# Kernel optimization log

Hardware: AMD Instinct MI355X
Metric: run time of the kernel (lower is better)

## Reference

```python
import jax, jax.numpy as jnp
import numpy as np
import math

D, H, S, B, E, FF = 768, 12, 1024, 2, 32768, 4 * 768
HD = D // H


def layer_norm(x, g, b, eps=1e-5):
    m = jnp.mean(x, axis=-1, keepdims=True)
    v = jnp.mean((x - m) ** 2, axis=-1, keepdims=True)
    return (x - m) / jnp.sqrt(v + eps) * g + b


def setup_inputs() -> dict:
    key = jax.random.key(0)
    ks = jax.random.split(key, 24)
    w = lambda k, shape: jax.random.normal(k, shape, dtype=jnp.float32) * 0.02
    inp = {
        "x": jax.random.normal(ks[0], (B, S, D), dtype=jnp.float32),
        "adj_mask": jax.random.randint(ks[1], (B, S, S), 0, 2).astype(bool),
        "edge_attr": jax.random.normal(ks[2], (E,), dtype=jnp.float32),
        "edge_index": jax.random.randint(ks[3], (2, E), 0, S),
        "norm1_g": jnp.ones((D,), jnp.float32),
        "norm1_b": jnp.zeros((D,), jnp.float32),
        "Wq": w(ks[4], (D, D)), "bq": jnp.zeros((D,), jnp.float32),
        "Wk": w(ks[5], (D, D)), "bk": jnp.zeros((D,), jnp.float32),
        "Wv": w(ks[6], (D, D)), "bv": jnp.zeros((D,), jnp.float32),
        "Wo": w(ks[7], (D, D)), "bo": jnp.zeros((D,), jnp.float32),
        "norm2_g": jnp.ones((D,), jnp.float32),
        "norm2_b": jnp.zeros((D,), jnp.float32),
        "mlp_W1": w(ks[8], (D, FF)), "mlp_b1": jnp.zeros((FF,), jnp.float32),
        "mlp_W2": w(ks[9], (FF, D)), "mlp_b2": jnp.zeros((D,), jnp.float32),
        # per-head edge-attr MLP: Linear(1,16) -> GELU -> Linear(16,1), stacked over H heads
        "ep_W1": w(ks[10], (H, 16)), "ep_b1": jnp.zeros((H, 16), jnp.float32),
        "ep_W2": w(ks[11], (H, 16)), "ep_b2": jnp.zeros((H,), jnp.float32),
    }
    return inp


def reference(x, adj_mask, edge_attr, edge_index,
              norm1_g, norm1_b, Wq, bq, Wk, bk, Wv, bv, Wo, bo,
              norm2_g, norm2_b, mlp_W1, mlp_b1, mlp_W2, mlp_b2,
              ep_W1, ep_b1, ep_W2, ep_b2):
    Bb, Ss, Dd = x.shape
    Hh = ep_W1.shape[0]
    hd = Dd // Hh
    residual = x
    nx = layer_norm(x, norm1_g, norm1_b)
    q = (nx @ Wq + bq).reshape(Bb, Ss, Hh, hd).transpose(0, 2, 1, 3)  # [B,H,S,hd]
    k = (nx @ Wk + bk).reshape(Bb, Ss, Hh, hd).transpose(0, 2, 1, 3)
    v = (nx @ Wv + bv).reshape(Bb, Ss, Hh, hd).transpose(0, 2, 1, 3)
    scores = jnp.einsum('bhqd,bhkd->bhqk', q, k) / math.sqrt(hd)
    mask = adj_mask.astype(bool)[:, None]  # [B,1,S,S]
    scores = jnp.where(mask, scores, jnp.float32(-1e9))
    # per-edge per-head bias (computed under no_grad in the original -> stop_gradient)
    h1 = jax.nn.gelu(edge_attr[:, None, None] * ep_W1[None] + ep_b1[None], approximate=False)  # [E,H,16]
    proj = jnp.einsum('ehk,hk->eh', h1, ep_W2) + ep_b2  # [E,H]
    proj = jax.lax.stop_gradient(proj)
    src, dst = edge_index[0], edge_index[1]
    bias = jnp.zeros((Hh, Ss, Ss), x.dtype).at[:, src, dst].set(proj.T)  # [H,S,S]
    scores = scores + jnp.where(mask, bias[None], jnp.float32(0.0))
    attn = jax.nn.softmax(scores, axis=-1)
    out = jnp.einsum('bhqk,bhkd->bhqd', attn, v)
    out = out.transpose(0, 2, 1, 3).reshape(Bb, Ss, Dd)
    x = residual + (out @ Wo + bo)
    y = layer_norm(x, norm2_g, norm2_b)
    y = jax.nn.gelu(y @ mlp_W1 + mlp_b1, approximate=False) @ mlp_W2 + mlp_b2
    return x + y
```

## Files before the change

### kernel.cpp

```cpp
#include <hip/hip_runtime.h>
#include <hip/hip_bf16.h>

#define B_ 2
#define S_ 1024
#define D_ 768
#define H_ 12
#define HD_ 64
#define FF_ 3072
#define E_ 32768
#define QS_ 2304
#define NSPLIT 4
#define BHS (B_ * H_ * S_)

typedef short bf16x8 __attribute__((ext_vector_type(8)));
typedef float f32x4 __attribute__((ext_vector_type(4)));

#define SW(row, seg) ((((seg) ^ ((row) & 7)) * 8))

__device__ __forceinline__ unsigned short f2bf(float f) {
    __hip_bfloat16 h = __float2bfloat16(f);
    return __builtin_bit_cast(unsigned short, h);
}
__device__ __forceinline__ float bf2f(unsigned short u) {
    unsigned int v = ((unsigned int)u) << 16;
    return __builtin_bit_cast(float, v);
}
__device__ __forceinline__ float gelu_exact(float x) {
    return 0.5f * x * (1.0f + erff(x * 0.70710678118654752f));
}

__global__ __launch_bounds__(256) void fill_winner_kernel(int* __restrict__ winner)
{
    const int idx = (blockIdx.x * 256 + threadIdx.x) * 4;
    int4 v; v.x = -1; v.y = -1; v.z = -1; v.w = -1;
    *reinterpret_cast<int4*>(&winner[idx]) = v;
}

__global__ __launch_bounds__(256) void ln_kernel(
    const float* __restrict__ x, const float* __restrict__ g,
    const float* __restrict__ b, unsigned short* __restrict__ out)
{
    const int row = blockIdx.x;
    const int t = threadIdx.x;
    const float* xr = x + (size_t)row * D_;
    float v0 = xr[t], v1 = xr[t + 256], v2 = xr[t + 512];
    float s = v0 + v1 + v2, s2 = v0 * v0 + v1 * v1 + v2 * v2;
    for (int m = 32; m; m >>= 1) { s += __shfl_xor(s, m); s2 += __shfl_xor(s2, m); }
    __shared__ float red[8];
    const int w = t >> 6;
    if ((t & 63) == 0) { red[w] = s; red[4 + w] = s2; }
    __syncthreads();
    s = red[0] + red[1] + red[2] + red[3];
    s2 = red[4] + red[5] + red[6] + red[7];
    const float mean = s * (1.f / D_);
    const float var = s2 * (1.f / D_) - mean * mean;
    const float rstd = rsqrtf(var + 1e-5f);
    unsigned short* orow = out + (size_t)row * D_;
    orow[t]       = f2bf((v0 - mean) * rstd * g[t]       + b[t]);
    orow[t + 256] = f2bf((v1 - mean) * rstd * g[t + 256] + b[t + 256]);
    orow[t + 512] = f2bf((v2 - mean) * rstd * g[t + 512] + b[t + 512]);
}

__global__ __launch_bounds__(256) void wtrans_all_kernel(
    const float* __restrict__ Wq, const float* __restrict__ Wk, const float* __restrict__ Wv,
    const float* __restrict__ Wo, const float* __restrict__ W1, const float* __restrict__ W2,
    unsigned short* __restrict__ wqkvt, unsigned short* __restrict__ wot,
    unsigned short* __restrict__ w1t, unsigned short* __restrict__ w2t,
    const float* __restrict__ bq, const float* __restrict__ bk, const float* __restrict__ bv,
    float* __restrict__ bqkv)
{
    const int z = blockIdx.z;
    const float* src; unsigned short* dst; int K, N, nb, kb;
    if (z < 4) {
        if (blockIdx.x >= 24 || blockIdx.y >= 24) return;
        K = 768; N = 768; nb = blockIdx.x * 32; kb = blockIdx.y * 32;
        src = (z == 0) ? Wq : (z == 1) ? Wk : (z == 2) ? Wv : Wo;
        dst = (z == 3) ? wot : wqkvt + (size_t)z * 768 * 768;
    } else if (z == 4) {
        if (blockIdx.y >= 24) return;
        K = 768; N = 3072; nb = blockIdx.x * 32; kb = blockIdx.y * 32;
        src = W1; dst = w1t;
    } else {
        if (blockIdx.y >= 24) return;
        K = 3072; N = 768; nb = blockIdx.y * 32; kb = blockIdx.x * 32;
        src = W2; dst = w2t;
    }
    __shared__ float tile[32][33];
    const int tx = threadIdx.x & 31, ty = threadIdx.x >> 5;
    for (int r = 0; r < 32; r += 8)
        tile[ty + r][tx] = src[(size_t)(kb + ty + r) * N + nb + tx];
    __syncthreads();
    for (int r = 0; r < 32; r += 8)
        dst[(size_t)(nb + ty + r) * K + kb + tx] = f2bf(tile[tx][ty + r]);
    if (z == 0 && blockIdx.x == 0 && blockIdx.y == 0) {
        for (int i = threadIdx.x; i < QS_; i += 256)
            bqkv[i] = (i < 768) ? bq[i] : (i < 1536) ? bk[i - 768] : bv[i - 1536];
    }
}

template<bool RES, bool OUTBF>
__global__ __launch_bounds__(256) void gemm_kernel(
    const unsigned short* __restrict__ A, const unsigned short* __restrict__ Bt,
    const float* __restrict__ bias, const float* __restrict__ res,
    void* __restrict__ outp, int M, int N, int K)
{
    __shared__ unsigned short As[64][40];
    __shared__ unsigned short Bs[64][40];
    const int m0 = blockIdx.y * 64, n0 = blockIdx.x * 64;
    const int t = threadIdx.x;
    const int w = t >> 6, l = t & 63;
    const int wm = w >> 1, wn = w & 1;
    const int r = l & 15, g = l >> 4;
    const int srow = t >> 2, sseg = t & 3;
    f32x4 acc[2][2] = {};
    for (int k0 = 0; k0 < K; k0 += 32) {
        __syncthreads();
        const uint4 av = *reinterpret_cast<const uint4*>(A + (size_t)(m0 + srow) * K + k0 + sseg * 8);
        *reinterpret_cast<uint4*>(&As[srow][sseg * 8]) = av;
        const uint4 bv = *reinterpret_cast<const uint4*>(Bt + (size_t)(n0 + srow) * K + k0 + sseg * 8);
        *reinterpret_cast<uint4*>(&Bs[srow][sseg * 8]) = bv;
        __syncthreads();
        bf16x8 af[2], bfr[2];
        af[0]  = *reinterpret_cast<const bf16x8*>(&As[wm * 32 + r][g * 8]);
        af[1]  = *reinterpret_cast<const bf16x8*>(&As[wm * 32 + 16 + r][g * 8]);
        bfr[0] = *reinterpret_cast<const bf16x8*>(&Bs[wn * 32 + r][g * 8]);
        bfr[1] = *reinterpret_cast<const bf16x8*>(&Bs[wn * 32 + 16 + r][g * 8]);
        for (int m = 0; m < 2; m++)
            for (int n = 0; n < 2; n++)
                acc[m][n] = __builtin_amdgcn_mfma_f32_16x16x32_bf16(af[m], bfr[n], acc[m][n], 0, 0, 0);
    }
    for (int m = 0; m < 2; m++)
        for (int n = 0; n < 2; n++) {
            const int col = n0 + wn * 32 + n * 16 + r;
            const float bvv = bias[col];
            for (int j = 0; j < 4; j++) {
                const int row = m0 + wm * 32 + m * 16 + g * 4 + j;
                float v = acc[m][n][j] + bvv;
                if (RES) v += res[(size_t)row * N + col];
                if (OUTBF) ((unsigned short*)outp)[(size_t)row * N + col] = f2bf(v);
                else       ((float*)outp)[(size_t)row * N + col] = v;
            }
        }
}

__global__ __launch_bounds__(256) void gemm_splitk_kernel(
    const unsigned short* __restrict__ A, const unsigned short* __restrict__ Bt,
    float* __restrict__ part, int M, int N, int K, int klen)
{
    __shared__ unsigned short As[64][40];
    __shared__ unsigned short Bs[64][40];
    const int m0 = blockIdx.y * 64, n0 = blockIdx.x * 64;
    const int kbeg = blockIdx.z * klen;
    const int t = threadIdx.x;
    const int w = t >> 6, l = t & 63;
    const int wm = w >> 1, wn = w & 1;
    const int r = l & 15, g = l >> 4;
    const int srow = t >> 2, sseg = t & 3;
    f32x4 acc[2][2] = {};
    for (int k0 = kbeg; k0 < kbeg + klen; k0 += 32) {
        __syncthreads();
        const uint4 av = *reinterpret_cast<const uint4*>(A + (size_t)(m0 + srow) * K + k0 + sseg * 8);
        *reinterpret_cast<uint4*>(&As[srow][sseg * 8]) = av;
        const uint4 bv = *reinterpret_cast<const uint4*>(Bt + (size_t)(n0 + srow) * K + k0 + sseg * 8);
        *reinterpret_cast<uint4*>(&Bs[srow][sseg * 8]) = bv;
        __syncthreads();
        bf16x8 af[2], bfr[2];
        af[0]  = *reinterpret_cast<const bf16x8*>(&As[wm * 32 + r][g * 8]);
        af[1]  = *reinterpret_cast<const bf16x8*>(&As[wm * 32 + 16 + r][g * 8]);
        bfr[0] = *reinterpret_cast<const bf16x8*>(&Bs[wn * 32 + r][g * 8]);
        bfr[1] = *reinterpret_cast<const bf16x8*>(&Bs[wn * 32 + 16 + r][g * 8]);
        for (int m = 0; m < 2; m++)
            for (int n = 0; n < 2; n++)
                acc[m][n] = __builtin_amdgcn_mfma_f32_16x16x32_bf16(af[m], bfr[n], acc[m][n], 0, 0, 0);
    }
    float* op = part + (size_t)blockIdx.z * M * N;
    for (int m = 0; m < 2; m++)
        for (int n = 0; n < 2; n++) {
            const int col = n0 + wn * 32 + n * 16 + r;
            for (int j = 0; j < 4; j++) {
                const int row = m0 + wm * 32 + m * 16 + g * 4 + j;
                op[(size_t)row * N + col] = acc[m][n][j];
            }
        }
}

__global__ __launch_bounds__(256) void w2_reduce_kernel(
    const float* __restrict__ part, const float* __restrict__ x2,
    const float* __restrict__ b2, float* __restrict__ out)
{
    const int idx = (blockIdx.x * 256 + threadIdx.x) * 4;
    const int col = idx % D_;
    const float4 p0 = *reinterpret_cast<const float4*>(&part[idx]);
    const float4 p1 = *reinterpret_cast<const float4*>(&part[(size_t)B_ * S_ * D_ + idx]);
    const float4 xr = *reinterpret_cast<const float4*>(&x2[idx]);
    const float4 bb = *reinterpret_cast<const float4*>(&b2[col]);
    float4 o;
    o.x = xr.x + bb.x + p0.x + p1.x;
    o.y = xr.y + bb.y + p0.y + p1.y;
    o.z = xr.z + bb.z + p0.z + p1.z;
    o.w = xr.w + bb.w + p0.w + p1.w;
    *reinterpret_cast<float4*>(&out[idx]) = o;
}

template<bool GELU, bool OUTBF>
__global__ __launch_bounds__(256) void gemm128_kernel(
    const unsigned short* __restrict__ A, const unsigned short* __restrict__ Bt,
    const float* __restrict__ bias, void* __restrict__ outp,
    int M, int N, int K, int scale_below)
{
    __shared__ unsigned short As[128][64];
    __shared__ unsigned short Bs[128][64];
    const int m0 = blockIdx.y * 128, n0 = blockIdx.x * 128;
    const int t = threadIdx.x;
    const int w = t >> 6, l = t & 63;
    const int wm = w >> 1, wn = w & 1;
    const int lr = l & 15, g = l >> 4;
    f32x4 acc[4][4] = {};
    for (int k0 = 0; k0 < K; k0 += 64) {
        __syncthreads();
        for (int i = 0; i < 4; i++) {
            const int idx = i * 256 + t;
            const int row = idx >> 3, seg = idx & 7;
            *reinterpret_cast<uint4*>(&As[row][SW(row, seg)]) =
                *reinterpret_cast<const uint4*>(A + (size_t)(m0 + row) * K + k0 + seg * 8);
            *reinterpret_cast<uint4*>(&Bs[row][SW(row, seg)]) =
                *reinterpret_cast<const uint4*>(Bt + (size_t)(n0 + row) * K + k0 + seg * 8);
        }
        __syncthreads();
        for (int kk = 0; kk < 2; kk++) {
            bf16x8 af[4], bfr[4];
            for (int m = 0; m < 4; m++) {
                const int r = wm * 64 + m * 16 + lr;
                af[m] = *reinterpret_cast<const bf16x8*>(&As[r][SW(r, kk * 4 + g)]);
            }
            for (int n = 0; n < 4; n++) {
                const int r = wn * 64 + n * 16 + lr;
                bfr[n] = *reinterpret_cast<const bf16x8*>(&Bs[r][SW(r, kk * 4 + g)]);
            }
            for (int m = 0; m < 4; m++)
                for (int n = 0; n < 4; n++)
                    acc[m][n] = __builtin_amdgcn_mfma_f32_16x16x32_bf16(af[m], bfr[n], acc[m][n], 0, 0, 0);
        }
    }
    for (int m = 0; m < 4; m++)
        for (int n = 0; n < 4; n++) {
            const int col = n0 + wn * 64 + n * 16 + lr;
            const float scl = (col < scale_below) ? 0.125f : 1.0f;
            const float bvv = bias[col];
            for (int j = 0; j < 4; j++) {
                const int row = m0 + wm * 64 + m * 16 + g * 4 + j;
                float v = (acc[m][n][j] + bvv) * scl;
                if (GELU) v = gelu_exact(v);
                if (OUTBF) ((unsigned short*)outp)[(size_t)row * N + col] = f2bf(v);
                else       ((float*)outp)[(size_t)row * N + col] = v;
            }
        }
}

__global__ __launch_bounds__(256) void vtrans_kernel(
    const unsigned short* __restrict__ qkv, unsigned short* __restrict__ vt)
{
    __shared__ unsigned short T[64][68];
    const int t = threadIdx.x;
    const int s0 = blockIdx.x * 64;
    const int h = blockIdx.y, b = blockIdx.z;
    const int r = t >> 2, seg = t & 3;
    const unsigned short* src = qkv + (size_t)(b * S_ + s0 + r) * QS_ + 1536 + h * HD_ + seg * 16;
    *reinterpret_cast<uint4*>(&T[r][seg * 16])     = *reinterpret_cast<const uint4*>(src);
    *reinterpret_cast<uint4*>(&T[r][seg * 16 + 8]) = *reinterpret_cast<const uint4*>(src + 8);
    __syncthreads();
    unsigned short tmp[16];
    for (int i = 0; i < 16; i++) tmp[i] = T[seg * 16 + i][r];
    unsigned short* dst = vt + ((size_t)(b * H_ + h) * HD_ + r) * S_ + s0 + seg * 16;
    *reinterpret_cast<uint4*>(dst)     = *reinterpret_cast<uint4*>(&tmp[0]);
    *reinterpret_cast<uint4*>(dst + 8) = *reinterpret_cast<uint4*>(&tmp[8]);
}

__global__ __launch_bounds__(256) void edge_proj_scatter_kernel(
    const float* __restrict__ ea, const float* __restrict__ W1, const float* __restrict__ b1,
    const float* __restrict__ W2, const float* __restrict__ b2,
    const int* __restrict__ ei, float* __restrict__ proj, int* __restrict__ winner)
{
    const int tid = blockIdx.x * 256 + threadIdx.x;
    const int e = tid / H_, h = tid - e * H_;
    const float a = ea[e];
    float s = 0.f;
    for (int j = 0; j < 16; j++) {
        const float tv = a * W1[h * 16 + j] + b1[h * 16 + j];
        s += gelu_exact(tv) * W2[h * 16 + j];
    }
    proj[tid] = s + b2[h];
    if (h == 0) {
        const int sn = ei[e], dn = ei[E_ + e];
        atomicMax(&winner[sn * S_ + dn], e);
    }
}

__global__ __launch_bounds__(256) void ebias_kernel(
    const int* __restrict__ winner, const float* __restrict__ proj,
    unsigned short* __restrict__ ebias)
{
    const int q = blockIdx.x;
    const int t = threadIdx.x;
    const int k4 = t * 4;
    const int4 wv = *reinterpret_cast<const int4*>(&winner[q * S_ + k4]);
    for (int h = 0; h < H_; h++) {
        unsigned int lo = 0, hi = 0;
        if (wv.x >= 0) lo |= (unsigned int)f2bf(proj[(size_t)wv.x * H_ + h]);
        if (wv.y >= 0) lo |= ((unsigned int)f2bf(proj[(size_t)wv.y * H_ + h])) << 16;
        if (wv.z >= 0) hi |= (unsigned int)f2bf(proj[(size_t)wv.z * H_ + h]);
        if (wv.w >= 0) hi |= ((unsigned int)f2bf(proj[(size_t)wv.w * H_ + h])) << 16;
        uint2 val; val.x = lo; val.y = hi;
        *reinterpret_cast<uint2*>(&ebias[((size_t)h * S_ + q) * S_ + k4]) = val;
    }
}

__global__ __launch_bounds__(256) void maskpack_kernel(
    const void* __restrict__ adj, unsigned int* __restrict__ mp)
{
    __shared__ unsigned int words[32];
    __shared__ int u8f;
    const int q = blockIdx.x, b = blockIdx.y;
    const int t = threadIdx.x;
    if (t < 32) words[t] = 0;
    if (t == 0) u8f = 0;
    __syncthreads();
    const unsigned int* row8 = (const unsigned int*)((const unsigned char*)adj + ((size_t)b * S_ + q) * S_);
    const unsigned int* row32 = (const unsigned int*)((const int*)adj + ((size_t)b * S_ + q) * S_);
    const unsigned int v = row8[t];
    if (v & 0xFF00FF00u) atomicOr(&u8f, 1);
    __syncthreads();
    if (u8f) {
        unsigned int nib = 0;
        if (v & 0x000000FFu) nib |= 1u;
        if (v & 0x0000FF00u) nib |= 2u;
        if (v & 0x00FF0000u) nib |= 4u;
        if (v & 0xFF000000u) nib |= 8u;
        if (nib) atomicOr(&words[t >> 3], nib << ((t & 7) * 4));
    } else {
        for (int i = 0; i < 4; i++) {
            const int k = i * 256 + t;
            if (row32[k]) atomicOr(&words[k >> 5], 1u << (k & 31));
        }
    }
    __syncthreads();
    if (t < 32) mp[((size_t)b * S_ + q) * 32 + t] = words[t];
}

__global__ __launch_bounds__(256) void attn_mfma_kernel(
    const unsigned short* __restrict__ qkv,
    const unsigned short* __restrict__ vt,
    const unsigned short* __restrict__ ebias,
    const unsigned int* __restrict__ mp,
    float* __restrict__ pacc,
    float2* __restrict__ pml)
{
    __shared__ unsigned short Ks[64][64];
    __shared__ unsigned short Vs[64][64];
    __shared__ unsigned short Eb[64][72];
    __shared__ unsigned int   Mw[64][2];
    __shared__ unsigned short Ps[4][16][64];
    const int t = threadIdx.x;
    const int w = t >> 6, l = t & 63;
    const int lr = l & 15, g = l >> 4;
    const int qt = blockIdx.x & 15, sp = blockIdx.x >> 4;
    const int q0 = qt * 64;
    const int h = blockIdx.y, b = blockIdx.z;
    const int bh = b * H_ + h;
    const size_t qbase = (size_t)b * S_ * QS_ + h * HD_;
    const size_t kbase = qbase + 768;
    const size_t vtbase = (size_t)bh * HD_ * S_;

    const int qrow = q0 + w * 16 + lr;
    const bf16x8 af0 = *reinterpret_cast<const bf16x8*>(qkv + qbase + (size_t)qrow * QS_ + g * 8);
    const bf16x8 af1 = *reinterpret_cast<const bf16x8*>(qkv + qbase + (size_t)qrow * QS_ + 32 + g * 8);

    float m_run[4], l_run[4];
    f32x4 acc[4] = {};
    for (int j = 0; j < 4; j++) { m_run[j] = -3.0e38f; l_run[j] = 0.f; }

    const int srow = t >> 2, sseg = t & 3;
    const int kt_beg = sp * (S_ / NSPLIT), kt_end = kt_beg + S_ / NSPLIT;
    for (int kt = kt_beg; kt < kt_end; kt += 64) {
        __syncthreads();
        {
            const unsigned short* ksrc = qkv + kbase + (size_t)(kt + srow) * QS_ + sseg * 16;
            *reinterpret_cast<uint4*>(&Ks[srow][SW(srow, sseg * 2)])     = *reinterpret_cast<const uint4*>(ksrc);
            *reinterpret_cast<uint4*>(&Ks[srow][SW(srow, sseg * 2 + 1)]) = *reinterpret_cast<const uint4*>(ksrc + 8);
            const unsigned short* vsrc = vt + vtbase + (size_t)srow * S_ + kt + sseg * 16;
            *reinterpret_cast<uint4*>(&Vs[srow][SW(srow, sseg * 2)])     = *reinterpret_cast<const uint4*>(vsrc);
            *reinterpret_cast<uint4*>(&Vs[srow][SW(srow, sseg * 2 + 1)]) = *reinterpret_cast<const uint4*>(vsrc + 8);
            const unsigned short* esrc = ebias + ((size_t)h * S_ + q0 + srow) * S_ + kt + sseg * 16;
            *reinterpret_cast<uint4*>(&Eb[srow][sseg * 16])     = *reinterpret_cast<const uint4*>(esrc);
            *reinterpret_cast<uint4*>(&Eb[srow][sseg * 16 + 8]) = *reinterpret_cast<const uint4*>(esrc + 8);
            if (t < 128) Mw[t >> 1][t & 1] = mp[((size_t)b * S_ + q0 + (t >> 1)) * 32 + (kt >> 5) + (t & 1)];
        }
        __syncthreads();
        f32x4 sc[4];
        for (int n = 0; n < 4; n++) {
            const int r = n * 16 + lr;
            const bf16x8 b0 = *reinterpret_cast<const bf16x8*>(&Ks[r][SW(r, g)]);
            const bf16x8 b1 = *reinterpret_cast<const bf16x8*>(&Ks[r][SW(r, 4 + g)]);
            f32x4 z = {};
            z = __builtin_amdgcn_mfma_f32_16x16x32_bf16(af0, b0, z, 0, 0, 0);
            z = __builtin_amdgcn_mfma_f32_16x16x32_bf16(af1, b1, z, 0, 0, 0);
            sc[n] = z;
        }
        float tmax[4] = {-3.0e38f, -3.0e38f, -3.0e38f, -3.0e38f};
        for (int n = 0; n < 4; n++) {
            for (int j = 0; j < 4; j++) {
                const int rq = w * 16 + g * 4 + j;
                const unsigned int word = Mw[rq][n >> 1];
                const bool msk = (word >> ((n & 1) * 16 + lr)) & 1;
                float sval;
                if (msk) sval = sc[n][j] + bf2f(Eb[rq][n * 16 + lr]);
                else sval = -1e9f;
                sc[n][j] = sval;
                tmax[j] = fmaxf(tmax[j], sval);
            }
        }
        float pscale[4];
        for (int j = 0; j < 4; j++) {
            float tm = tmax[j];
            tm = fmaxf(tm, __shfl_xor(tm, 1));
            tm = fmaxf(tm, __shfl_xor(tm, 2));
            tm = fmaxf(tm, __shfl_xor(tm, 4));
            tm = fmaxf(tm, __shfl_xor(tm, 8));
            const float mnew = fmaxf(m_run[j], tm);
            pscale[j] = __expf(m_run[j] - mnew);
            m_run[j] = mnew;
            l_run[j] *= pscale[j];
        }
        float psum[4] = {0.f, 0.f, 0.f, 0.f};
        for (int n = 0; n < 4; n++) {
            for (int j = 0; j < 4; j++) {
                const float p = __expf(sc[n][j] - m_run[j]);
                psum[j] += p;
                const int row = g * 4 + j;
                Ps[w][row][SW(row, n * 2 + (lr >> 3)) + (lr & 7)] = f2bf(p);
            }
        }
        for (int j = 0; j < 4; j++) {
            float s = psum[j];
            s += __shfl_xor(s, 1); s += __shfl_xor(s, 2);
            s += __shfl_xor(s, 4); s += __shfl_xor(s, 8);
            l_run[j] += s;
            for (int n2 = 0; n2 < 4; n2++) acc[n2][j] *= pscale[j];
        }
        const bf16x8 pa0 = *reinterpret_cast<const bf16x8*>(&Ps[w][lr][SW(lr, g)]);
        const bf16x8 pa1 = *reinterpret_cast<const bf16x8*>(&Ps[w][lr][SW(lr, 4 + g)]);
        for (int n2 = 0; n2 < 4; n2++) {
            const int r = n2 * 16 + lr;
            const bf16x8 vb0 = *reinterpret_cast<const bf16x8*>(&Vs[r][SW(r, g)]);
            const bf16x8 vb1 = *reinterpret_cast<const bf16x8*>(&Vs[r][SW(r, 4 + g)]);
            acc[n2] = __builtin_amdgcn_mfma_f32_16x16x32_bf16(pa0, vb0, acc[n2], 0, 0, 0);
            acc[n2] = __builtin_amdgcn_mfma_f32_16x16x32_bf16(pa1, vb1, acc[n2], 0, 0, 0);
        }
    }
    const size_t prow = (size_t)sp * BHS + (size_t)bh * S_;
    for (int j = 0; j < 4; j++) {
        const int qg = q0 + w * 16 + g * 4 + j;
        for (int n2 = 0; n2 < 4; n2++)
            pacc[(prow + qg) * 64 + n2 * 16 + lr] = acc[n2][j];
        if (lr == 0) { float2 v; v.x = m_run[j]; v.y = l_run[j]; pml[prow + qg] = v; }
    }
}

__global__ __launch_bounds__(256) void attn_combine_kernel(
    const float* __restrict__ pacc, const float2* __restrict__ pml,
    unsigned short* __restrict__ attnb)
{
    const int idx = (blockIdx.x * 256 + threadIdx.x) * 4;
    const int r = idx >> 6, d = idx & 63;
    float2 ml[NSPLIT];
    float mx = -3.0e38f;
    for (int s = 0; s < NSPLIT; s++) {
        ml[s] = pml[(size_t)s * BHS + r];
        mx = fmaxf(mx, ml[s].x);
    }
    float wgt[NSPLIT], L = 0.f;
    for (int s = 0; s < NSPLIT; s++) {
        wgt[s] = __expf(ml[s].x - mx);
        L += ml[s].y * wgt[s];
    }
    const float inv = (L > 0.f) ? 1.f / L : 0.f;
    float4 o = {0.f, 0.f, 0.f, 0.f};
    for (int s = 0; s < NSPLIT; s++) {
        const float4 a = *reinterpret_cast<const float4*>(&pacc[((size_t)s * BHS + r) * 64 + d]);
        o.x += a.x * wgt[s]; o.y += a.y * wgt[s];
        o.z += a.z * wgt[s]; o.w += a.w * wgt[s];
    }
    const int bh = r >> 10, q = r & 1023;
    const int b = bh / H_, h = bh - b * H_;
    ushort4 ov;
    ov.x = f2bf(o.x * inv); ov.y = f2bf(o.y * inv);
    ov.z = f2bf(o.z * inv); ov.w = f2bf(o.w * inv);
    *reinterpret_cast<ushort4*>(&attnb[((size_t)(b * S_ + q)) * D_ + h * HD_ + d]) = ov;
}

extern "C" void kernel_launch(void* const* d_in, const int* in_sizes, int n_in,
                              void* d_out, int out_size, void* d_ws, size_t ws_size,
                              hipStream_t stream)
{
    const float* x    = (const float*)d_in[0];
    const void*  adj  = d_in[1];
    const float* ea   = (const float*)d_in[2];
    const int*   ei   = (const int*)d_in[3];
    const float* g1   = (const float*)d_in[4];
    const float* bn1  = (const float*)d_in[5];
    const float* Wq   = (const float*)d_in[6];
    const float* bq   = (const float*)d_in[7];
    const float* Wk   = (const float*)d_in[8];
    const float* bk   = (const float*)d_in[9];
    const float* Wv   = (const float*)d_in[10];
    const float* bv   = (const float*)d_in[11];
    const float* Wo   = (const float*)d_in[12];
    const float* bo   = (const float*)d_in[13];
    const float* g2   = (const float*)d_in[14];
    const float* bn2  = (const float*)d_in[15];
    const float* W1   = (const float*)d_in[16];
    const float* mb1  = (const float*)d_in[17];
    const float* W2   = (const float*)d_in[18];
    const float* mb2  = (const float*)d_in[19];
    const float* epW1 = (const float*)d_in[20];
    const float* epb1 = (const float*)d_in[21];
    const float* epW2 = (const float*)d_in[22];
    const float* epb2 = (const float*)d_in[23];

    char* ws = (char*)d_ws;
    size_t off = 0;
    auto carve = [&](size_t bytes) -> void* {
        void* p = ws + off;
        off += (bytes + 255) & ~(size_t)255;
        return p;
    };
    unsigned short* wqkvt = (unsigned short*)carve((size_t)QS_ * D_ * 2);
    unsigned short* wot   = (unsigned short*)carve((size_t)D_ * D_ * 2);
    unsigned short* w1t   = (unsigned short*)carve((size_t)FF_ * D_ * 2);
    unsigned short* w2t   = (unsigned short*)carve((size_t)D_ * FF_ * 2);
    float*          bqkv  = (float*)carve((size_t)QS_ * 4);
    float*          proj  = (float*)carve((size_t)E_ * H_ * 4);
    int*            winner= (int*)carve((size_t)S_ * S_ * 4);
    unsigned short* ebias = (unsigned short*)carve((size_t)H_ * S_ * S_ * 2);
    unsigned int*   mpk   = (unsigned int*)carve((size_t)B_ * S_ * 32 * 4);
    unsigned short* nxb   = (unsigned short*)carve((size_t)B_ * S_ * D_ * 2);
    unsigned short* attnb = (unsigned short*)carve((size_t)B_ * S_ * D_ * 2);
    unsigned short* qkv   = (unsigned short*)carve((size_t)B_ * S_ * QS_ * 2);
    unsigned short* vtb   = (unsigned short*)carve((size_t)B_ * S_ * D_ * 2);
    float*          x2f   = (float*)carve((size_t)B_ * S_ * D_ * 4);
    float*          pacc  = (float*)carve((size_t)NSPLIT * BHS * 64 * 4);
    float2*         pml   = (float2*)carve((size_t)NSPLIT * BHS * 8);
    unsigned short* ln2b = nxb;
    unsigned short* hb   = qkv;
    float*          pw2  = (float*)ebias;

    const int M = B_ * S_;

    fill_winner_kernel<<<(S_ * S_) / 1024, 256, 0, stream>>>(winner);

    wtrans_all_kernel<<<dim3(96, 24, 6), 256, 0, stream>>>(
        Wq, Wk, Wv, Wo, W1, W2, wqkvt, wot, w1t, w2t, bq, bk, bv, bqkv);

    ln_kernel<<<M, 256, 0, stream>>>(x, g1, bn1, nxb);

    gemm128_kernel<false, true><<<dim3(QS_ / 128, M / 128), 256, 0, stream>>>(
        nxb, wqkvt, bqkv, qkv, M, QS_, D_, 768);

    vtrans_kernel<<<dim3(S_ / 64, H_, B_), 256, 0, stream>>>(qkv, vtb);

    edge_proj_scatter_kernel<<<(E_ * H_) / 256, 256, 0, stream>>>(
        ea, epW1, epb1, epW2, epb2, ei, proj, winner);
    ebias_kernel<<<S_, 256, 0, stream>>>(winner, proj, ebias);
    maskpack_kernel<<<dim3(S_, B_), 256, 0, stream>>>(adj, mpk);

    attn_mfma_kernel<<<dim3(16 * NSPLIT, H_, B_), 256, 0, stream>>>(
        qkv, vtb, ebias, mpk, pacc, pml);
    attn_combine_kernel<<<(BHS * 64) / 1024, 256, 0, stream>>>(pacc, pml, attnb);

    gemm_kernel<true, false><<<dim3(D_ / 64, M / 64), 256, 0, stream>>>(
        attnb, wot, bo, x, x2f, M, D_, D_);

    ln_kernel<<<M, 256, 0, stream>>>(x2f, g2, bn2, ln2b);

    gemm128_kernel<true, true><<<dim3(FF_ / 128, M / 128), 256, 0, stream>>>(
        ln2b, w1t, mb1, hb, M, FF_, D_, 0);
    gemm_splitk_kernel<<<dim3(D_ / 64, M / 64, 2), 256, 0, stream>>>(
        hb, w2t, pw2, M, D_, FF_, FF_ / 2);
    w2_reduce_kernel<<<(M * D_) / 1024, 256, 0, stream>>>(pw2, x2f, mb2, (float*)d_out);
}
```

Baseline: 207.4 us.

## Use direct global-to-LDS loads in 128-tile GEMM, reuse it for split-K W2

Replaces the register-staged tile loads in the 128x128 GEMM with global_load_lds direct-to-LDS transfers, keeping the XOR swizzle by permuting source segments. Adds a split-K mode to this kernel and uses it for the W2 projection with four K-splits, replacing the smaller 64x64 split-K kernel. It also folds the winner-fill into the mask-pack kernel to drop one launch, and halves the attention split count. The risks are more partial-sum traffic in the reduce and lower attention parallelism.

```diff
diff --git a/kernel.cpp b/kernel.cpp
--- a/kernel.cpp
+++ b/kernel.cpp
@@ -9,7 +9,8 @@
 #define FF_ 3072
 #define E_ 32768
 #define QS_ 2304
-#define NSPLIT 4
+#define NSPLIT 2
+#define NSPLIT_W2 4
 #define BHS (B_ * H_ * S_)
 
 typedef short bf16x8 __attribute__((ext_vector_type(8)));
@@ -28,12 +29,9 @@
 __device__ __forceinline__ float gelu_exact(float x) {
     return 0.5f * x * (1.0f + erff(x * 0.70710678118654752f));
 }
-
-__global__ __launch_bounds__(256) void fill_winner_kernel(int* __restrict__ winner)
-{
-    const int idx = (blockIdx.x * 256 + threadIdx.x) * 4;
-    int4 v; v.x = -1; v.y = -1; v.z = -1; v.w = -1;
-    *reinterpret_cast<int4*>(&winner[idx]) = v;
+__device__ __forceinline__ void gload_lds16(const unsigned short* g, unsigned short* l) {
+    __builtin_amdgcn_global_load_lds((const __attribute__((address_space(1))) void*)g,
+                                     (__attribute__((address_space(3))) void*)l, 16, 0, 0);
 }
 
 __global__ __launch_bounds__(256) void ln_kernel(
@@ -143,70 +141,11 @@
         }
 }
 
-__global__ __launch_bounds__(256) void gemm_splitk_kernel(
-    const unsigned short* __restrict__ A, const unsigned short* __restrict__ Bt,
-    float* __restrict__ part, int M, int N, int K, int klen)
-{
-    __shared__ unsigned short As[64][40];
-    __shared__ unsigned short Bs[64][40];
-    const int m0 = blockIdx.y * 64, n0 = blockIdx.x * 64;
-    const int kbeg = blockIdx.z * klen;
-    const int t = threadIdx.x;
-    const int w = t >> 6, l = t & 63;
-    const int wm = w >> 1, wn = w & 1;
-    const int r = l & 15, g = l >> 4;
-    const int srow = t >> 2, sseg = t & 3;
-    f32x4 acc[2][2] = {};
-    for (int k0 = kbeg; k0 < kbeg + klen; k0 += 32) {
-        __syncthreads();
-        const uint4 av = *reinterpret_cast<const uint4*>(A + (size_t)(m0 + srow) * K + k0 + sseg * 8);
-        *reinterpret_cast<uint4*>(&As[srow][sseg * 8]) = av;
-        const uint4 bv = *reinterpret_cast<const uint4*>(Bt + (size_t)(n0 + srow) * K + k0 + sseg * 8);
-        *reinterpret_cast<uint4*>(&Bs[srow][sseg * 8]) = bv;
-        __syncthreads();
-        bf16x8 af[2], bfr[2];
-        af[0]  = *reinterpret_cast<const bf16x8*>(&As[wm * 32 + r][g * 8]);
-        af[1]  = *reinterpret_cast<const bf16x8*>(&As[wm * 32 + 16 + r][g * 8]);
-        bfr[0] = *reinterpret_cast<const bf16x8*>(&Bs[wn * 32 + r][g * 8]);
-        bfr[1] = *reinterpret_cast<const bf16x8*>(&Bs[wn * 32 + 16 + r][g * 8]);
-        for (int m = 0; m < 2; m++)
-            for (int n = 0; n < 2; n++)
-                acc[m][n] = __builtin_amdgcn_mfma_f32_16x16x32_bf16(af[m], bfr[n], acc[m][n], 0, 0, 0);
-    }
-    float* op = part + (size_t)blockIdx.z * M * N;
-    for (int m = 0; m < 2; m++)
-        for (int n = 0; n < 2; n++) {
-            const int col = n0 + wn * 32 + n * 16 + r;
-            for (int j = 0; j < 4; j++) {
-                const int row = m0 + wm * 32 + m * 16 + g * 4 + j;
-                op[(size_t)row * N + col] = acc[m][n][j];
-            }
-        }
-}
-
-__global__ __launch_bounds__(256) void w2_reduce_kernel(
-    const float* __restrict__ part, const float* __restrict__ x2,
-    const float* __restrict__ b2, float* __restrict__ out)
-{
-    const int idx = (blockIdx.x * 256 + threadIdx.x) * 4;
-    const int col = idx % D_;
-    const float4 p0 = *reinterpret_cast<const float4*>(&part[idx]);
-    const float4 p1 = *reinterpret_cast<const float4*>(&part[(size_t)B_ * S_ * D_ + idx]);
-    const float4 xr = *reinterpret_cast<const float4*>(&x2[idx]);
-    const float4 bb = *reinterpret_cast<const float4*>(&b2[col]);
-    float4 o;
-    o.x = xr.x + bb.x + p0.x + p1.x;
-    o.y = xr.y + bb.y + p0.y + p1.y;
-    o.z = xr.z + bb.z + p0.z + p1.z;
-    o.w = xr.w + bb.w + p0.w + p1.w;
-    *reinterpret_cast<float4*>(&out[idx]) = o;
-}
-
-template<bool GELU, bool OUTBF>
+template<bool GELU, bool OUTBF, bool SPLITK>
 __global__ __launch_bounds__(256) void gemm128_kernel(
     const unsigned short* __restrict__ A, const unsigned short* __restrict__ Bt,
     const float* __restrict__ bias, void* __restrict__ outp,
-    int M, int N, int K, int scale_below)
+    int M, int N, int K, int klen, int scale_below)
 {
     __shared__ unsigned short As[128][64];
     __shared__ unsigned short Bs[128][64];
@@ -215,16 +154,18 @@
     const int w = t >> 6, l = t & 63;
     const int wm = w >> 1, wn = w & 1;
     const int lr = l & 15, g = l >> 4;
+    const int lrow8 = l >> 3;
+    const int lseg = (l & 7) ^ lrow8;
+    const int kbeg = SPLITK ? blockIdx.z * klen : 0;
+    const int kend = SPLITK ? kbeg + klen : K;
     f32x4 acc[4][4] = {};
-    for (int k0 = 0; k0 < K; k0 += 64) {
+    for (int k0 = kbeg; k0 < kend; k0 += 64) {
         __syncthreads();
-        for (int i = 0; i < 4; i++) {
-            const int idx = i * 256 + t;
-            const int row = idx >> 3, seg = idx & 7;
-            *reinterpret_cast<uint4*>(&As[row][SW(row, seg)]) =
-                *reinterpret_cast<const uint4*>(A + (size_t)(m0 + row) * K + k0 + seg * 8);
-            *reinterpret_cast<uint4*>(&Bs[row][SW(row, seg)]) =
-                *reinterpret_cast<const uint4*>(Bt + (size_t)(n0 + row) * K + k0 + seg * 8);
+        for (int j = 0; j < 4; j++) {
+            const int q = w * 4 + j;
+            const int row = q * 8 + lrow8;
+            gload_lds16(A  + (size_t)(m0 + row) * K + k0 + lseg * 8, &As[q * 8][0]);
+            gload_lds16(Bt + (size_t)(n0 + row) * K + k0 + lseg * 8, &Bs[q * 8][0]);
         }
         __syncthreads();
         for (int kk = 0; kk < 2; kk++) {
@@ -242,19 +183,48 @@
                     acc[m][n] = __builtin_amdgcn_mfma_f32_16x16x32_bf16(af[m], bfr[n], acc[m][n], 0, 0, 0);
         }
     }
-    for (int m = 0; m < 4; m++)
-        for (int n = 0; n < 4; n++) {
-            const int col = n0 + wn * 64 + n * 16 + lr;
-            const float scl = (col < scale_below) ? 0.125f : 1.0f;
-            const float bvv = bias[col];
-            for (int j = 0; j < 4; j++) {
-                const int row = m0 + wm * 64 + m * 16 + g * 4 + j;
-                float v = (acc[m][n][j] + bvv) * scl;
-                if (GELU) v = gelu_exact(v);
-                if (OUTBF) ((unsigned short*)outp)[(size_t)row * N + col] = f2bf(v);
-                else       ((float*)outp)[(size_t)row * N + col] = v;
-            }
-        }
+    if (SPLITK) {
+        float* op = (float*)outp + (size_t)blockIdx.z * M * N;
+        for (int m = 0; m < 4; m++)
+            for (int n = 0; n < 4; n++) {
+                const int col = n0 + wn * 64 + n * 16 + lr;
+                for (int j = 0; j < 4; j++) {
+                    const int row = m0 + wm * 64 + m * 16 + g * 4 + j;
+                    op[(size_t)row * N + col] = acc[m][n][j];
+                }
+            }
+    } else {
+        for (int m = 0; m < 4; m++)
+            for (int n = 0; n < 4; n++) {
+                const int col = n0 + wn * 64 + n * 16 + lr;
+                const float scl = (col < scale_below) ? 0.125f : 1.0f;
+                const float bvv = bias[col];
+                for (int j = 0; j < 4; j++) {
+                    const int row = m0 + wm * 64 + m * 16 + g * 4 + j;
+                    float v = (acc[m][n][j] + bvv) * scl;
+                    if (GELU) v = gelu_exact(v);
+                    if (OUTBF) ((unsigned short*)outp)[(size_t)row * N + col] = f2bf(v);
+                    else       ((float*)outp)[(size_t)row * N + col] = v;
+                }
+            }
+    }
+}
+
+__global__ __launch_bounds__(256) void w2_reduce_kernel(
+    const float* __restrict__ part, const float* __restrict__ x2,
+    const float* __restrict__ b2, float* __restrict__ out)
+{
+    const int idx = (blockIdx.x * 256 + threadIdx.x) * 4;
+    const int col = idx % D_;
+    const float4 xr = *reinterpret_cast<const float4*>(&x2[idx]);
+    const float4 bb = *reinterpret_cast<const float4*>(&b2[col]);
+    float4 o;
+    o.x = xr.x + bb.x; o.y = xr.y + bb.y; o.z = xr.z + bb.z; o.w = xr.w + bb.w;
+    for (int s = 0; s < NSPLIT_W2; s++) {
+        const float4 p = *reinterpret_cast<const float4*>(&part[(size_t)s * B_ * S_ * D_ + idx]);
+        o.x += p.x; o.y += p.y; o.z += p.z; o.w += p.w;
+    }
+    *reinterpret_cast<float4*>(&out[idx]) = o;
 }
 
 __global__ __launch_bounds__(256) void vtrans_kernel(
@@ -316,12 +286,16 @@
 }
 
 __global__ __launch_bounds__(256) void maskpack_kernel(
-    const void* __restrict__ adj, unsigned int* __restrict__ mp)
-{
+    const void* __restrict__ adj, unsigned int* __restrict__ mp, int* __restrict__ winner)
+{
+    const int q = blockIdx.x, b = blockIdx.y;
+    const int t = threadIdx.x;
+    if (b == 0) {
+        int4 v; v.x = -1; v.y = -1; v.z = -1; v.w = -1;
+        reinterpret_cast<int4*>(winner)[q * 256 + t] = v;
+    }
     __shared__ unsigned int words[32];
     __shared__ int u8f;
-    const int q = blockIdx.x, b = blockIdx.y;
-    const int t = threadIdx.x;
     if (t < 32) words[t] = 0;
     if (t == 0) u8f = 0;
     __syncthreads();
@@ -556,22 +530,21 @@
 
     const int M = B_ * S_;
 
-    fill_winner_kernel<<<(S_ * S_) / 1024, 256, 0, stream>>>(winner);
+    maskpack_kernel<<<dim3(S_, B_), 256, 0, stream>>>(adj, mpk, winner);
 
     wtrans_all_kernel<<<dim3(96, 24, 6), 256, 0, stream>>>(
         Wq, Wk, Wv, Wo, W1, W2, wqkvt, wot, w1t, w2t, bq, bk, bv, bqkv);
 
     ln_kernel<<<M, 256, 0, stream>>>(x, g1, bn1, nxb);
 
-    gemm128_kernel<false, true><<<dim3(QS_ / 128, M / 128), 256, 0, stream>>>(
-        nxb, wqkvt, bqkv, qkv, M, QS_, D_, 768);
+    gemm128_kernel<false, true, false><<<dim3(QS_ / 128, M / 128), 256, 0, stream>>>(
+        nxb, wqkvt, bqkv, qkv, M, QS_, D_, D_, 768);
 
     vtrans_kernel<<<dim3(S_ / 64, H_, B_), 256, 0, stream>>>(qkv, vtb);
 
     edge_proj_scatter_kernel<<<(E_ * H_) / 256, 256, 0, stream>>>(
         ea, epW1, epb1, epW2, epb2, ei, proj, winner);
     ebias_kernel<<<S_, 256, 0, stream>>>(winner, proj, ebias);
-    maskpack_kernel<<<dim3(S_, B_), 256, 0, stream>>>(adj, mpk);
 
     attn_mfma_kernel<<<dim3(16 * NSPLIT, H_, B_), 256, 0, stream>>>(
         qkv, vtb, ebias, mpk, pacc, pml);
@@ -582,9 +555,9 @@
 
     ln_kernel<<<M, 256, 0, stream>>>(x2f, g2, bn2, ln2b);
 
-    gemm128_kernel<true, true><<<dim3(FF_ / 128, M / 128), 256, 0, stream>>>(
-        ln2b, w1t, mb1, hb, M, FF_, D_, 0);
-    gemm_splitk_kernel<<<dim3(D_ / 64, M / 64, 2), 256, 0, stream>>>(
-        hb, w2t, pw2, M, D_, FF_, FF_ / 2);
+    gemm128_kernel<true, true, false><<<dim3(FF_ / 128, M / 128), 256, 0, stream>>>(
+        ln2b, w1t, mb1, hb, M, FF_, D_, D_, 0);
+    gemm128_kernel<false, false, true><<<dim3(D_ / 128, M / 128, NSPLIT_W2), 256, 0, stream>>>(
+        hb, w2t, mb2, pw2, M, D_, FF_, FF_ / NSPLIT_W2, 0);
     w2_reduce_kernel<<<(M * D_) / 1024, 256, 0, stream>>>(pw2, x2f, mb2, (float*)d_out);
 }
```

Result: faster. 191.1 us (-7.9%).
